# Optimization experiments

Hardware: AMD Instinct MI355X
Metric: run time of the kernel (lower is better)

Reference implementation:

```python
import jax, jax.numpy as jnp
import numpy as np

H = 512
V = 8000

def _attn(hidden, enc, W, b, v):
    # hidden: [1,B,H], enc: [T,B,H] -> context [1,B,H]
    encB = jnp.transpose(enc, (1, 0, 2))                      # [B,T,H]
    Hrep = jnp.broadcast_to(jnp.transpose(hidden, (1, 0, 2)), encB.shape)
    energy = jnp.tanh(jnp.concatenate([Hrep, encB], axis=-1) @ W.T + b)  # [B,T,H]
    scores = jnp.einsum('bth,h->bt', energy, v)               # [B,T]
    a = jax.nn.softmax(scores, axis=1)
    ctx = jnp.einsum('bt,bth->bh', a, encB)                   # [B,H]
    return ctx[None]

def _gru_step(x, h, W_ih, W_hh, b_ih, b_hh):
    # x: [B,in], h: [B,H]; PyTorch gate order r,z,n
    gi = x @ W_ih.T + b_ih
    gh = h @ W_hh.T + b_hh
    i_r, i_z, i_n = jnp.split(gi, 3, axis=1)
    h_r, h_z, h_n = jnp.split(gh, 3, axis=1)
    r = jax.nn.sigmoid(i_r + h_r)
    z = jax.nn.sigmoid(i_z + h_z)
    n = jnp.tanh(i_n + r * h_n)
    return (1.0 - z) * n + z * h

def setup_inputs() -> dict:
    key = jax.random.key(0)
    ks = jax.random.split(key, 20)
    B, Tz, Tu, E, D = 128, 64, 128, 512, 5
    gin = E + 2 * H + D  # 1541
    s = 0.02  # small init scale to keep tanh/sigmoid unsaturated
    return {
        'z_enc_out': jax.random.normal(ks[0], (Tz, B, H), jnp.float32),
        'u_enc_out': jax.random.normal(ks[1], (Tu, B, H), jnp.float32),
        'm_t_input': jax.random.randint(ks[2], (1, B), 0, V),
        'degree_input': jax.random.uniform(ks[3], (B, D), jnp.float32),
        'last_hidden': jax.random.normal(ks[4], (1, B, H), jnp.float32),
        'sparse_response': jax.random.uniform(ks[5], (B, Tz, V + Tz), jnp.float32, 1e-3, 1.0),
        'emb_table': jax.random.normal(ks[6], (V, E), jnp.float32) * s,
        'attn_z_W': jax.random.normal(ks[7], (H, 2 * H), jnp.float32) * s,
        'attn_z_b': jnp.zeros((H,), jnp.float32),
        'attn_z_v': jax.random.normal(ks[8], (H,), jnp.float32) * s,
        'attn_u_W': jax.random.normal(ks[9], (H, 2 * H), jnp.float32) * s,
        'attn_u_b': jnp.zeros((H,), jnp.float32),
        'attn_u_v': jax.random.normal(ks[10], (H,), jnp.float32) * s,
        'gru_W_ih': jax.random.normal(ks[11], (3 * H, gin), jnp.float32) * s,
        'gru_W_hh': jax.random.normal(ks[12], (3 * H, H), jnp.float32) * s,
        'gru_b_ih': jnp.zeros((3 * H,), jnp.float32),
        'gru_b_hh': jnp.zeros((3 * H,), jnp.float32),
        'proj_W': jax.random.normal(ks[13], (V, 3 * H), jnp.float32) * s,
        'proj_b': jnp.zeros((V,), jnp.float32),
        'copy2_W': jax.random.normal(ks[14], (H, H), jnp.float32) * s,
        'copy2_b': jnp.zeros((H,), jnp.float32),
    }

def reference(z_enc_out, u_enc_out, m_t_input, degree_input, last_hidden,
              sparse_response, emb_table, attn_z_W, attn_z_b, attn_z_v,
              attn_u_W, attn_u_b, attn_u_v, gru_W_ih, gru_W_hh, gru_b_ih,
              gru_b_hh, proj_W, proj_b, copy2_W, copy2_b):
    m_embed = emb_table[m_t_input]                                 # [1,B,E]
    z_ctx = _attn(last_hidden, z_enc_out, attn_z_W, attn_z_b, attn_z_v)  # [1,B,H]
    u_ctx = _attn(last_hidden, u_enc_out, attn_u_W, attn_u_b, attn_u_v)  # [1,B,H]
    gru_in = jnp.concatenate([m_embed, u_ctx, z_ctx, degree_input[None]], axis=2)
    h_new = _gru_step(gru_in[0], last_hidden[0], gru_W_ih, gru_W_hh, gru_b_ih, gru_b_hh)  # [B,H]
    gru_out = h_new[None]                                          # [1,B,H]
    gen_score = (jnp.concatenate([z_ctx, u_ctx, gru_out], axis=2)[0] @ proj_W.T + proj_b)  # [B,V]
    # copy scores over z encoder positions
    zT = jnp.transpose(z_enc_out, (1, 0, 2))                       # [B,Tz,H]
    cs = jnp.tanh(zT @ copy2_W.T + copy2_b)                        # [B,Tz,H]
    z_score = jnp.einsum('bth,bh->bt', cs, h_new)                  # [B,Tz]
    m = jnp.max(z_score, axis=1, keepdims=True)
    e = jnp.exp(z_score - m)
    z_copy = jnp.log(jnp.einsum('bt,btv->bv', e, sparse_response)) + m  # [B,V+Tz]
    scores = jax.nn.softmax(jnp.concatenate([gen_score, z_copy], axis=1), axis=1)
    gen, cp = scores[:, :V], scores[:, V:]
    proba = jnp.concatenate([gen + cp[:, :V], cp[:, V:]], axis=1)  # [B,V+Tz]
    return proba, gru_out, gru_out
```

## Files before the change

### kernel.cpp

```cpp
#include <hip/hip_runtime.h>
#include <hip/hip_bf16.h>
#include <math.h>

#define B_   128
#define H_   512
#define TZ   64
#define TU   128
#define V_   8000
#define VC   8064
#define GIN  1541
#define GINP 1568
#define G3   1536
#define NB   8

typedef float f32x4 __attribute__((ext_vector_type(4)));
typedef __bf16 bf16x8 __attribute__((ext_vector_type(8)));

__device__ __forceinline__ float sigmoidf_(float x){ return 1.f/(1.f+__expf(-x)); }

__device__ __forceinline__ void cvt8(const float* __restrict__ s, __bf16* __restrict__ d){
  float4 x = *(const float4*)s;
  float4 y = *(const float4*)(s+4);
  bf16x8 r;
  r[0]=(__bf16)x.x; r[1]=(__bf16)x.y; r[2]=(__bf16)x.z; r[3]=(__bf16)x.w;
  r[4]=(__bf16)y.x; r[5]=(__bf16)y.y; r[6]=(__bf16)y.z; r[7]=(__bf16)y.w;
  *(bf16x8*)d = r;
}

#define U_Z   524288u
#define U_U   1048576u
#define U_H   8192u
#define U_ZW  65536u
#define U_UW  65536u
#define U_CW  32768u
#define U_WHH 98304u
#define U_PW  1536000u
#define U_WIH 301056u
#define CVT_UNITS (U_Z+U_U+U_H+U_ZW+U_UW+U_CW+U_WHH+U_PW+U_WIH)

__global__ __launch_bounds__(256) void cvt_all(
    const float* __restrict__ z, const float* __restrict__ u, const float* __restrict__ hid,
    const float* __restrict__ zW, const float* __restrict__ uW, const float* __restrict__ cW,
    const float* __restrict__ whh, const float* __restrict__ pW, const float* __restrict__ wih,
    __bf16* __restrict__ zb, __bf16* __restrict__ ub, __bf16* __restrict__ hb,
    __bf16* __restrict__ zWb, __bf16* __restrict__ uWb, __bf16* __restrict__ cWb,
    __bf16* __restrict__ whhb, __bf16* __restrict__ pWb, __bf16* __restrict__ Wp)
{
  unsigned t = blockIdx.x*256u + threadIdx.x;
  if (t >= CVT_UNITS) return;
  unsigned o = t;
  if (o >= CVT_UNITS - U_WIH) {
    o -= (CVT_UNITS - U_WIH);
    unsigned r = o / (GINP/8), cu = o % (GINP/8);
    int c0 = cu*8;
    const float* src = wih + (size_t)r*GIN;
    bf16x8 v;
#pragma unroll
    for (int e = 0; e < 8; ++e) {
      int c = c0 + e;
      v[e] = (__bf16)((c < GIN) ? src[c] : 0.f);
    }
    *(bf16x8*)(Wp + (size_t)r*GINP + c0) = v;
    return;
  }
  const float* s; __bf16* d;
  if      (o < U_Z)                   { s=z;   d=zb;   }
  else if ((o-=U_Z)   < U_U)          { s=u;   d=ub;   }
  else if ((o-=U_U)   < U_H)          { s=hid; d=hb;   }
  else if ((o-=U_H)   < U_ZW)         { s=zW;  d=zWb;  }
  else if ((o-=U_ZW)  < U_UW)         { s=uW;  d=uWb;  }
  else if ((o-=U_UW)  < U_CW)         { s=cW;  d=cWb;  }
  else if ((o-=U_CW)  < U_WHH)        { s=whh; d=whhb; }
  else     { o-=U_WHH;                  s=pW;  d=pWb;  }
  cvt8(s + (size_t)o*8, d + (size_t)o*8);
}

__global__ __launch_bounds__(256) void hidden3(
    const __bf16* __restrict__ hb,
    const __bf16* __restrict__ zWb, const float* __restrict__ zbias, float* __restrict__ hWz,
    const __bf16* __restrict__ uWb, const float* __restrict__ ubias, float* __restrict__ hWu,
    const __bf16* __restrict__ whhb, const float* __restrict__ hbias, float* __restrict__ gh)
{
  const int wv = threadIdx.x >> 6, lane = threadIdx.x & 63;
  const int tile = blockIdx.x*4 + wv;
  if (tile >= 80) return;
  const __bf16* W; const float* bias; float* C; int ldw, ldc, nbn, lt;
  if (tile < 16)      { W=zWb;  bias=zbias; C=hWz; ldw=2*H_; ldc=H_; nbn=8;  lt=tile; }
  else if (tile < 32) { W=uWb;  bias=ubias; C=hWu; ldw=2*H_; ldc=H_; nbn=8;  lt=tile-16; }
  else                { W=whhb; bias=hbias; C=gh;  ldw=H_;   ldc=G3; nbn=24; lt=tile-32; }
  const int bn = (lt % nbn) * 64, bm = (lt / nbn) * 64;
  const int col = lane & 15, g = lane >> 4;
  f32x4 acc[4][4] = {};
  for (int k0 = 0; k0 < 512; k0 += 32) {
    const int k = k0 + g*8;
    bf16x8 af[4], bw[4];
#pragma unroll
    for (int i = 0; i < 4; ++i) {
      af[i] = *(const bf16x8*)(hb + (size_t)(bm + i*16 + col)*H_ + k);
      bw[i] = *(const bf16x8*)(W  + (size_t)(bn + i*16 + col)*ldw + k);
    }
#pragma unroll
    for (int i = 0; i < 4; ++i)
#pragma unroll
      for (int j = 0; j < 4; ++j)
        acc[i][j] = __builtin_amdgcn_mfma_f32_16x16x32_bf16(af[i], bw[j], acc[i][j], 0, 0, 0);
  }
#pragma unroll
  for (int mi = 0; mi < 4; ++mi)
#pragma unroll
    for (int r = 0; r < 4; ++r) {
      int m = bm + mi*16 + g*4 + r;
#pragma unroll
      for (int ni = 0; ni < 4; ++ni) {
        int n = bn + ni*16 + col;
        C[(size_t)m*ldc + n] = acc[mi][ni][r] + bias[n];
      }
    }
}

__global__ __launch_bounds__(256) void mfma_energy2(
    const __bf16* __restrict__ Az, const __bf16* __restrict__ Wz, int ldwz,
    const float* __restrict__ addz, int asz, const float* __restrict__ mulz, int msz,
    float* __restrict__ outz, int Tz,
    const __bf16* __restrict__ Au, const __bf16* __restrict__ Wu, int ldwu,
    const float* __restrict__ addu, int asu, const float* __restrict__ mulu, int msu,
    float* __restrict__ outu, int Tu,
    int ztiles, int ntiles)
{
  const int wv = threadIdx.x >> 6, lane = threadIdx.x & 63;
  const int tile = blockIdx.x*4 + wv;
  if (tile >= ntiles) return;
  const __bf16 *A, *W; const float *add, *mul; float* outp;
  int ldw, as, ms, T, lt;
  if (tile < ztiles) { A=Az; W=Wz; ldw=ldwz; add=addz; as=asz; mul=mulz; ms=msz; outp=outz; T=Tz; lt=tile; }
  else               { A=Au; W=Wu; ldw=ldwu; add=addu; as=asu; mul=mulu; ms=msu; outp=outu; T=Tu; lt=tile-ztiles; }
  const int nb = lt & 7;
  const int bn = nb * 64, bm = (lt >> 3) * 64;
  const int col = lane & 15, g = lane >> 4;
  f32x4 acc[4][4] = {};
  for (int k0 = 0; k0 < 512; k0 += 32) {
    const int k = k0 + g*8;
    bf16x8 af[4], bw[4];
#pragma unroll
    for (int i = 0; i < 4; ++i) {
      af[i] = *(const bf16x8*)(A + (size_t)(bm + i*16 + col)*512 + k);
      bw[i] = *(const bf16x8*)(W + (size_t)(bn + i*16 + col)*ldw + k);
    }
#pragma unroll
    for (int i = 0; i < 4; ++i)
#pragma unroll
      for (int j = 0; j < 4; ++j)
        acc[i][j] = __builtin_amdgcn_mfma_f32_16x16x32_bf16(af[i], bw[j], acc[i][j], 0, 0, 0);
  }
#pragma unroll
  for (int mi = 0; mi < 4; ++mi)
#pragma unroll
    for (int r = 0; r < 4; ++r) {
      int m = bm + mi*16 + g*4 + r;
      int b = m & (B_-1), t = m >> 7;
      float p = 0.f;
#pragma unroll
      for (int ni = 0; ni < 4; ++ni) {
        int n = bn + ni*16 + col;
        float v = tanhf(acc[mi][ni][r] + add[(size_t)b*as + n]);
        p += v * mul[(size_t)b*ms + n];
      }
      p += __shfl_xor(p, 1); p += __shfl_xor(p, 2);
      p += __shfl_xor(p, 4); p += __shfl_xor(p, 8);
      if (col == 0) outp[(size_t)nb*(B_*T) + b*T + t] = p;
    }
}

__global__ __launch_bounds__(256) void attn_ctx_concat(
    const float* __restrict__ partZ, const float* __restrict__ partU,
    const __bf16* __restrict__ zb, const __bf16* __restrict__ ub,
    const int* __restrict__ m_t, const float* __restrict__ emb,
    const float* __restrict__ degree,
    __bf16* __restrict__ gin, __bf16* __restrict__ cat3b)
{
  const int b = blockIdx.x, tid = threadIdx.x;
  __shared__ float sa[256];
  __shared__ float awz[TZ];
  __shared__ float awu[TU];
  {
    float s = -INFINITY;
    if (tid < TZ) {
      s = 0.f;
#pragma unroll
      for (int nb = 0; nb < NB; ++nb) s += partZ[(size_t)nb*(B_*TZ) + b*TZ + tid];
    }
    sa[tid] = s; __syncthreads();
    for (int o = 128; o > 0; o >>= 1) { if (tid < o) sa[tid] = fmaxf(sa[tid], sa[tid+o]); __syncthreads(); }
    float mx = sa[0]; __syncthreads();
    float e = (tid < TZ) ? __expf(s - mx) : 0.f;
    sa[tid] = e; __syncthreads();
    for (int o = 128; o > 0; o >>= 1) { if (tid < o) sa[tid] += sa[tid+o]; __syncthreads(); }
    float inv = 1.f / sa[0];
    if (tid < TZ) awz[tid] = e * inv;
    __syncthreads();
  }
  {
    float s = -INFINITY;
    if (tid < TU) {
      s = 0.f;
#pragma unroll
      for (int nb = 0; nb < NB; ++nb) s += partU[(size_t)nb*(B_*TU) + b*TU + tid];
    }
    sa[tid] = s; __syncthreads();
    for (int o = 128; o > 0; o >>= 1) { if (tid < o) sa[tid] = fmaxf(sa[tid], sa[tid+o]); __syncthreads(); }
    float mx = sa[0]; __syncthreads();
    float e = (tid < TU) ? __expf(s - mx) : 0.f;
    sa[tid] = e; __syncthreads();
    for (int o = 128; o > 0; o >>= 1) { if (tid < o) sa[tid] += sa[tid+o]; __syncthreads(); }
    float inv = 1.f / sa[0];
    if (tid < TU) awu[tid] = e * inv;
    __syncthreads();
  }
  const float* e = emb + (size_t)m_t[b] * H_;
  for (int h = tid; h < H_; h += 256) {
    float accz = 0.f, accu = 0.f;
    for (int t = 0; t < TZ; ++t) accz += awz[t] * (float)zb[((size_t)t*B_ + b)*H_ + h];
    for (int t = 0; t < TU; ++t) accu += awu[t] * (float)ub[((size_t)t*B_ + b)*H_ + h];
    gin[(size_t)b*GINP + h]          = (__bf16)e[h];
    gin[(size_t)b*GINP + H_ + h]     = (__bf16)accu;
    gin[(size_t)b*GINP + 2*H_ + h]   = (__bf16)accz;
    cat3b[(size_t)b*G3 + h]          = (__bf16)accz;
    cat3b[(size_t)b*G3 + H_ + h]     = (__bf16)accu;
  }
  if (tid < 5) gin[(size_t)b*GINP + 3*H_ + tid] = (__bf16)degree[b*5 + tid];
  if (tid >= 5 && tid < 32) gin[(size_t)b*GINP + GIN + (tid-5)] = (__bf16)0.f;
}

__global__ __launch_bounds__(256) void mfma_gru(
    const __bf16* __restrict__ A, const __bf16* __restrict__ W,
    float* __restrict__ giA, float* __restrict__ giB)
{
  const int wv = threadIdx.x >> 6, lane = threadIdx.x & 63;
  const int tile = blockIdx.x*4 + wv;
  if (tile >= 96) return;
  const int half = tile / 48, lt = tile % 48;
  const int bn = (lt % 24) * 64, bm = (lt / 24) * 64;
  const int col = lane & 15, g = lane >> 4;
  const int kbeg = half ? 800 : 0, kend_ = half ? GINP : 800;
  float* C = half ? giB : giA;
  f32x4 acc[4][4] = {};
  for (int k0 = kbeg; k0 < kend_; k0 += 32) {
    const int k = k0 + g*8;
    bf16x8 af[4], bw[4];
#pragma unroll
    for (int i = 0; i < 4; ++i) {
      af[i] = *(const bf16x8*)(A + (size_t)(bm + i*16 + col)*GINP + k);
      bw[i] = *(const bf16x8*)(W + (size_t)(bn + i*16 + col)*GINP + k);
    }
#pragma unroll
    for (int i = 0; i < 4; ++i)
#pragma unroll
      for (int j = 0; j < 4; ++j)
        acc[i][j] = __builtin_amdgcn_mfma_f32_16x16x32_bf16(af[i], bw[j], acc[i][j], 0, 0, 0);
  }
#pragma unroll
  for (int mi = 0; mi < 4; ++mi)
#pragma unroll
    for (int r = 0; r < 4; ++r) {
      int m = bm + mi*16 + g*4 + r;
#pragma unroll
      for (int ni = 0; ni < 4; ++ni)
        C[(size_t)m*G3 + bn + ni*16 + col] = acc[mi][ni][r];
    }
}

__global__ __launch_bounds__(256) void gru_kernel(
    const float* __restrict__ giA, const float* __restrict__ giB,
    const float* __restrict__ gh, const float* __restrict__ bih,
    const float* __restrict__ hprev,
    float* __restrict__ hnew, __bf16* __restrict__ cat3b,
    float* __restrict__ out1, float* __restrict__ out2)
{
  int idx = blockIdx.x*256 + threadIdx.x;
  int b = idx >> 9, h = idx & (H_-1);
  size_t base = (size_t)b*G3;
  float ir = giA[base + h]        + giB[base + h]        + bih[h]        + gh[base + h];
  float iz = giA[base + H_ + h]   + giB[base + H_ + h]   + bih[H_ + h]   + gh[base + H_ + h];
  float in_= giA[base + 2*H_ + h] + giB[base + 2*H_ + h] + bih[2*H_ + h];
  float hn = gh[base + 2*H_ + h];
  float r = sigmoidf_(ir);
  float z = sigmoidf_(iz);
  float n = tanhf(in_ + r*hn);
  float hv = (1.f - z)*n + z*hprev[idx];
  hnew[idx] = hv;
  cat3b[base + 2*H_ + h] = (__bf16)hv;
  out1[idx] = hv;
  out2[idx] = hv;
}

__global__ __launch_bounds__(256) void proj_copy(
    const __bf16* __restrict__ cat3b, const __bf16* __restrict__ pWb, float* __restrict__ P,
    const __bf16* __restrict__ zb, const __bf16* __restrict__ cWb,
    const float* __restrict__ c2b, const float* __restrict__ hnew,
    float* __restrict__ partC)
{
  const int wv = threadIdx.x >> 6, lane = threadIdx.x & 63;
  const int tile = blockIdx.x*4 + wv;
  const int col = lane & 15, g = lane >> 4;
  if (tile < 750) {
    const int s = tile / 250, t2 = tile % 250;
    const int bn = (t2 % 125) * 64, bm = (t2 / 125) * 64;
    const __bf16* As = cat3b + s*512;
    const __bf16* Ws = pWb + s*512;
    float* C = P + (size_t)s*B_*V_;
    f32x4 acc[4][4] = {};
    for (int k0 = 0; k0 < 512; k0 += 32) {
      const int k = k0 + g*8;
      bf16x8 af[4], bw[4];
#pragma unroll
      for (int i = 0; i < 4; ++i) {
        af[i] = *(const bf16x8*)(As + (size_t)(bm + i*16 + col)*G3 + k);
        bw[i] = *(const bf16x8*)(Ws + (size_t)(bn + i*16 + col)*G3 + k);
      }
#pragma unroll
      for (int i = 0; i < 4; ++i)
#pragma unroll
        for (int j = 0; j < 4; ++j)
          acc[i][j] = __builtin_amdgcn_mfma_f32_16x16x32_bf16(af[i], bw[j], acc[i][j], 0, 0, 0);
    }
#pragma unroll
    for (int mi = 0; mi < 4; ++mi)
#pragma unroll
      for (int r = 0; r < 4; ++r) {
        int m = bm + mi*16 + g*4 + r;
#pragma unroll
        for (int ni = 0; ni < 4; ++ni)
          C[(size_t)m*V_ + bn + ni*16 + col] = acc[mi][ni][r];
      }
  } else if (tile < 750 + 1024) {
    const int lt = tile - 750;
    const int nb = lt & 7;
    const int bn = nb * 64, bm = (lt >> 3) * 64;
    f32x4 acc[4][4] = {};
    for (int k0 = 0; k0 < 512; k0 += 32) {
      const int k = k0 + g*8;
      bf16x8 af[4], bw[4];
#pragma unroll
      for (int i = 0; i < 4; ++i) {
        af[i] = *(const bf16x8*)(zb + (size_t)(bm + i*16 + col)*512 + k);
        bw[i] = *(const bf16x8*)(cWb + (size_t)(bn + i*16 + col)*H_ + k);
      }
#pragma unroll
      for (int i = 0; i < 4; ++i)
#pragma unroll
        for (int j = 0; j < 4; ++j)
          acc[i][j] = __builtin_amdgcn_mfma_f32_16x16x32_bf16(af[i], bw[j], acc[i][j], 0, 0, 0);
    }
#pragma unroll
    for (int mi = 0; mi < 4; ++mi)
#pragma unroll
      for (int r = 0; r < 4; ++r) {
        int m = bm + mi*16 + g*4 + r;
        int b = m & (B_-1), t = m >> 7;
        float p = 0.f;
#pragma unroll
        for (int ni = 0; ni < 4; ++ni) {
          int n = bn + ni*16 + col;
          float v = tanhf(acc[mi][ni][r] + c2b[n]);
          p += v * hnew[(size_t)b*H_ + n];
        }
        p += __shfl_xor(p, 1); p += __shfl_xor(p, 2);
        p += __shfl_xor(p, 4); p += __shfl_xor(p, 8);
        if (col == 0) partC[(size_t)nb*(B_*TZ) + b*TZ + t] = p;
      }
  }
}

__global__ __launch_bounds__(256) void zcopy_kernel(
    const float* __restrict__ partC, const float* __restrict__ sr,
    float* __restrict__ zbuf)
{
  const int b = blockIdx.y, tid = threadIdx.x;
  __shared__ float se[TZ];
  __shared__ float smx;
  if (tid < TZ) {
    float s = 0.f;
#pragma unroll
    for (int nb = 0; nb < NB; ++nb) s += partC[(size_t)nb*(B_*TZ) + b*TZ + tid];
    float mx = s;
    mx = fmaxf(mx, __shfl_xor(mx, 1));  mx = fmaxf(mx, __shfl_xor(mx, 2));
    mx = fmaxf(mx, __shfl_xor(mx, 4));  mx = fmaxf(mx, __shfl_xor(mx, 8));
    mx = fmaxf(mx, __shfl_xor(mx, 16)); mx = fmaxf(mx, __shfl_xor(mx, 32));
    se[tid] = __expf(s - mx);
    if (tid == 0) smx = mx;
  }
  __syncthreads();
  const int v0 = blockIdx.x*1024 + tid*4;
  if (v0 >= VC) return;
  float4 acc = {0.f, 0.f, 0.f, 0.f};
  const float* base = sr + (size_t)b*TZ*VC;
#pragma unroll 4
  for (int t = 0; t < TZ; ++t) {
    float et = se[t];
    float4 x = *(const float4*)(base + (size_t)t*VC + v0);
    acc.x += et*x.x; acc.y += et*x.y; acc.z += et*x.z; acc.w += et*x.w;
  }
  float m = smx;
  float* out = zbuf + (size_t)b*VC + v0;
  out[0] = __logf(acc.x) + m;
  out[1] = __logf(acc.y) + m;
  out[2] = __logf(acc.z) + m;
  out[3] = __logf(acc.w) + m;
}

__global__ __launch_bounds__(256) void final_softmax2(
    const float* __restrict__ p0, const float* __restrict__ p1, const float* __restrict__ p2,
    const float* __restrict__ bias, const float* __restrict__ zbuf, float* __restrict__ out0)
{
  const int b = blockIdx.x, tid = threadIdx.x;
  const float* q0 = p0 + (size_t)b*V_;
  const float* q1 = p1 + (size_t)b*V_;
  const float* q2 = p2 + (size_t)b*V_;
  const float* zr = zbuf + (size_t)b*VC;
  __shared__ float sa[256];
  float mx = -INFINITY;
  for (int i = tid; i < V_; i += 256) mx = fmaxf(mx, q0[i]+q1[i]+q2[i]+bias[i]);
  for (int i = tid; i < VC; i += 256) mx = fmaxf(mx, zr[i]);
  sa[tid] = mx; __syncthreads();
  for (int o = 128; o > 0; o >>= 1) { if (tid < o) sa[tid] = fmaxf(sa[tid], sa[tid+o]); __syncthreads(); }
  mx = sa[0]; __syncthreads();
  float sum = 0.f;
  for (int i = tid; i < V_; i += 256) sum += __expf(q0[i]+q1[i]+q2[i]+bias[i] - mx);
  for (int i = tid; i < VC; i += 256) sum += __expf(zr[i] - mx);
  sa[tid] = sum; __syncthreads();
  for (int o = 128; o > 0; o >>= 1) { if (tid < o) sa[tid] += sa[tid+o]; __syncthreads(); }
  float inv = 1.f / sa[0];
  float* o0 = out0 + (size_t)b*VC;
  for (int j = tid; j < V_; j += 256)
    o0[j] = (__expf(q0[j]+q1[j]+q2[j]+bias[j]-mx) + __expf(zr[j]-mx)) * inv;
  for (int j = tid; j < TZ; j += 256)
    o0[V_ + j] = __expf(zr[V_ + j] - mx) * inv;
}

extern "C" void kernel_launch(void* const* d_in, const int* in_sizes, int n_in,
                              void* d_out, int out_size, void* d_ws, size_t ws_size,
                              hipStream_t stream)
{
  const float* z_enc   = (const float*)d_in[0];
  const float* u_enc   = (const float*)d_in[1];
  const int*   m_t     = (const int*)  d_in[2];
  const float* degree  = (const float*)d_in[3];
  const float* hidden  = (const float*)d_in[4];
  const float* sr      = (const float*)d_in[5];
  const float* emb     = (const float*)d_in[6];
  const float* attn_z_W= (const float*)d_in[7];
  const float* attn_z_b= (const float*)d_in[8];
  const float* attn_z_v= (const float*)d_in[9];
  const float* attn_u_W= (const float*)d_in[10];
  const float* attn_u_b= (const float*)d_in[11];
  const float* attn_u_v= (const float*)d_in[12];
  const float* gru_W_ih= (const float*)d_in[13];
  const float* gru_W_hh= (const float*)d_in[14];
  const float* gru_b_ih= (const float*)d_in[15];
  const float* gru_b_hh= (const float*)d_in[16];
  const float* proj_W  = (const float*)d_in[17];
  const float* proj_b  = (const float*)d_in[18];
  const float* copy2_W = (const float*)d_in[19];
  const float* copy2_b = (const float*)d_in[20];

  float* out0 = (float*)d_out;
  float* out1 = out0 + (size_t)B_*VC;
  float* out2 = out1 + (size_t)B_*H_;

  float* ws    = (float*)d_ws;
  float* hWz   = ws;
  float* hWu   = hWz   + B_*H_;
  float* gh    = hWu   + B_*H_;
  float* partZ = gh    + B_*G3;
  float* partU = partZ + NB*B_*TZ;
  float* partC = partU + NB*B_*TU;
  float* giA   = partC + NB*B_*TZ;
  float* giB   = giA   + B_*G3;
  float* hnew  = giB   + B_*G3;
  float* p0    = hnew  + B_*H_;
  float* p1    = p0    + (size_t)B_*V_;
  float* p2    = p1    + (size_t)B_*V_;
  float* zbuf  = p2    + (size_t)B_*V_;
  __bf16* gin   = (__bf16*)(zbuf + (size_t)B_*VC);
  __bf16* Wp    = gin   + (size_t)B_*GINP;
  __bf16* zb    = Wp    + (size_t)G3*GINP;
  __bf16* ub    = zb    + (size_t)TZ*B_*H_;
  __bf16* hb    = ub    + (size_t)TU*B_*H_;
  __bf16* zWb   = hb    + (size_t)B_*H_;
  __bf16* uWb   = zWb   + (size_t)H_*2*H_;
  __bf16* cWb   = uWb   + (size_t)H_*2*H_;
  __bf16* whhb  = cWb   + (size_t)H_*H_;
  __bf16* pWb   = whhb  + (size_t)G3*H_;
  __bf16* cat3b = pWb   + (size_t)V_*G3;

  cvt_all<<<(CVT_UNITS + 255)/256, 256, 0, stream>>>(
      z_enc, u_enc, hidden, attn_z_W, attn_u_W, copy2_W, gru_W_hh, proj_W, gru_W_ih,
      zb, ub, hb, zWb, uWb, cWb, whhb, pWb, Wp);

  hidden3<<<20, 256, 0, stream>>>(hb, zWb, attn_z_b, hWz, uWb, attn_u_b, hWu, whhb, gru_b_hh, gh);

  mfma_energy2<<<768, 256, 0, stream>>>(
      zb, zWb + H_, 2*H_, hWz, H_, attn_z_v, 0, partZ, TZ,
      ub, uWb + H_, 2*H_, hWu, H_, attn_u_v, 0, partU, TU,
      1024, 3072);

  attn_ctx_concat<<<B_, 256, 0, stream>>>(partZ, partU, zb, ub, m_t, emb, degree, gin, cat3b);

  mfma_gru<<<24, 256, 0, stream>>>(gin, Wp, giA, giB);
  gru_kernel<<<(B_*H_)/256, 256, 0, stream>>>(giA, giB, gh, gru_b_ih, hidden, hnew, cat3b, out1, out2);

  proj_copy<<<444, 256, 0, stream>>>(cat3b, pWb, p0, zb, cWb, copy2_b, hnew, partC);

  zcopy_kernel<<<dim3((VC + 1023)/1024, B_), 256, 0, stream>>>(partC, sr, zbuf);

  final_softmax2<<<B_, 256, 0, stream>>>(p0, p1, p2, proj_b, zbuf, out0);
}
```

Measured before the change: 295.2 us.

## Drop proj_W bf16 pre-conversion, stage energy A tiles in LDS, online softmax

Removes the separate fp32-to-bf16 conversion of the large projection weight and instead converts it inline while loading inside proj_copy. Each projection wave now covers all 128 batch rows, so every weight element is read once. The attention energy kernel stages a 64-row A tile in swizzled LDS that four waves share across 8 column blocks, cutting redundant global reads. The final softmax now makes a single online max/sum pass instead of separate max and sum passes. The trade-offs are more registers per wave in proj_copy (8x4 accumulators) and fewer waves in flight.

```diff
diff --git a/kernel.cpp b/kernel.cpp
--- a/kernel.cpp
+++ b/kernel.cpp
@@ -18,13 +18,16 @@
 
 __device__ __forceinline__ float sigmoidf_(float x){ return 1.f/(1.f+__expf(-x)); }
 
-__device__ __forceinline__ void cvt8(const float* __restrict__ s, __bf16* __restrict__ d){
-  float4 x = *(const float4*)s;
-  float4 y = *(const float4*)(s+4);
+__device__ __forceinline__ bf16x8 load8_bf16(const float* __restrict__ p){
+  float4 x = *(const float4*)p;
+  float4 y = *(const float4*)(p+4);
   bf16x8 r;
   r[0]=(__bf16)x.x; r[1]=(__bf16)x.y; r[2]=(__bf16)x.z; r[3]=(__bf16)x.w;
   r[4]=(__bf16)y.x; r[5]=(__bf16)y.y; r[6]=(__bf16)y.z; r[7]=(__bf16)y.w;
-  *(bf16x8*)d = r;
+  return r;
+}
+__device__ __forceinline__ void cvt8(const float* __restrict__ s, __bf16* __restrict__ d){
+  *(bf16x8*)d = load8_bf16(s);
 }
 
 #define U_Z   524288u
@@ -34,17 +37,16 @@
 #define U_UW  65536u
 #define U_CW  32768u
 #define U_WHH 98304u
-#define U_PW  1536000u
 #define U_WIH 301056u
-#define CVT_UNITS (U_Z+U_U+U_H+U_ZW+U_UW+U_CW+U_WHH+U_PW+U_WIH)
+#define CVT_UNITS (U_Z+U_U+U_H+U_ZW+U_UW+U_CW+U_WHH+U_WIH)
 
 __global__ __launch_bounds__(256) void cvt_all(
     const float* __restrict__ z, const float* __restrict__ u, const float* __restrict__ hid,
     const float* __restrict__ zW, const float* __restrict__ uW, const float* __restrict__ cW,
-    const float* __restrict__ whh, const float* __restrict__ pW, const float* __restrict__ wih,
+    const float* __restrict__ whh, const float* __restrict__ wih,
     __bf16* __restrict__ zb, __bf16* __restrict__ ub, __bf16* __restrict__ hb,
     __bf16* __restrict__ zWb, __bf16* __restrict__ uWb, __bf16* __restrict__ cWb,
-    __bf16* __restrict__ whhb, __bf16* __restrict__ pWb, __bf16* __restrict__ Wp)
+    __bf16* __restrict__ whhb, __bf16* __restrict__ Wp)
 {
   unsigned t = blockIdx.x*256u + threadIdx.x;
   if (t >= CVT_UNITS) return;
@@ -70,8 +72,7 @@
   else if ((o-=U_H)   < U_ZW)         { s=zW;  d=zWb;  }
   else if ((o-=U_ZW)  < U_UW)         { s=uW;  d=uWb;  }
   else if ((o-=U_UW)  < U_CW)         { s=cW;  d=cWb;  }
-  else if ((o-=U_CW)  < U_WHH)        { s=whh; d=whhb; }
-  else     { o-=U_WHH;                  s=pW;  d=pWb;  }
+  else     { o-=U_CW;                   s=whh; d=whhb; }
   cvt8(s + (size_t)o*8, d + (size_t)o*8);
 }
 
@@ -118,57 +119,72 @@
     }
 }
 
-__global__ __launch_bounds__(256) void mfma_energy2(
-    const __bf16* __restrict__ Az, const __bf16* __restrict__ Wz, int ldwz,
-    const float* __restrict__ addz, int asz, const float* __restrict__ mulz, int msz,
-    float* __restrict__ outz, int Tz,
-    const __bf16* __restrict__ Au, const __bf16* __restrict__ Wu, int ldwu,
-    const float* __restrict__ addu, int asu, const float* __restrict__ mulu, int msu,
-    float* __restrict__ outu, int Tu,
-    int ztiles, int ntiles)
-{
-  const int wv = threadIdx.x >> 6, lane = threadIdx.x & 63;
-  const int tile = blockIdx.x*4 + wv;
-  if (tile >= ntiles) return;
-  const __bf16 *A, *W; const float *add, *mul; float* outp;
-  int ldw, as, ms, T, lt;
-  if (tile < ztiles) { A=Az; W=Wz; ldw=ldwz; add=addz; as=asz; mul=mulz; ms=msz; outp=outz; T=Tz; lt=tile; }
-  else               { A=Au; W=Wu; ldw=ldwu; add=addu; as=asu; mul=mulu; ms=msu; outp=outu; T=Tu; lt=tile-ztiles; }
-  const int nb = lt & 7;
-  const int bn = nb * 64, bm = (lt >> 3) * 64;
+__global__ __launch_bounds__(256) void energy_lds(
+    const __bf16* __restrict__ zb, const __bf16* __restrict__ zWe,
+    const float* __restrict__ hWz, const float* __restrict__ vz, float* __restrict__ partZ,
+    const __bf16* __restrict__ ub, const __bf16* __restrict__ uWe,
+    const float* __restrict__ hWu, const float* __restrict__ vu, float* __restrict__ partU)
+{
+  __shared__ __bf16 Asm[64*512];
+  const int blk = blockIdx.x;
+  const __bf16 *A, *W; const float *add, *vv; float* outp; int T, bm;
+  if (blk < 128) { A=zb; W=zWe; add=hWz; vv=vz; outp=partZ; T=TZ; bm=blk*64; }
+  else           { A=ub; W=uWe; add=hWu; vv=vu; outp=partU; T=TU; bm=(blk-128)*64; }
+  const int tid = threadIdx.x;
+  {
+    const int r4 = tid >> 6;
+    const int c8 = (tid & 63) * 8;
+#pragma unroll
+    for (int it = 0; it < 16; ++it) {
+      int row = it*4 + r4;
+      unsigned off = (unsigned)row*1024u + (unsigned)c8*2u;
+      off ^= ((unsigned)(row & 7) << 4);
+      *(bf16x8*)((char*)Asm + off) = *(const bf16x8*)(A + (size_t)(bm + row)*512 + c8);
+    }
+  }
+  __syncthreads();
+  const int wv = tid >> 6, lane = tid & 63;
   const int col = lane & 15, g = lane >> 4;
-  f32x4 acc[4][4] = {};
-  for (int k0 = 0; k0 < 512; k0 += 32) {
-    const int k = k0 + g*8;
-    bf16x8 af[4], bw[4];
-#pragma unroll
-    for (int i = 0; i < 4; ++i) {
-      af[i] = *(const bf16x8*)(A + (size_t)(bm + i*16 + col)*512 + k);
-      bw[i] = *(const bf16x8*)(W + (size_t)(bn + i*16 + col)*ldw + k);
-    }
-#pragma unroll
-    for (int i = 0; i < 4; ++i)
-#pragma unroll
-      for (int j = 0; j < 4; ++j)
-        acc[i][j] = __builtin_amdgcn_mfma_f32_16x16x32_bf16(af[i], bw[j], acc[i][j], 0, 0, 0);
-  }
-#pragma unroll
-  for (int mi = 0; mi < 4; ++mi)
-#pragma unroll
-    for (int r = 0; r < 4; ++r) {
-      int m = bm + mi*16 + g*4 + r;
-      int b = m & (B_-1), t = m >> 7;
-      float p = 0.f;
-#pragma unroll
-      for (int ni = 0; ni < 4; ++ni) {
-        int n = bn + ni*16 + col;
-        float v = tanhf(acc[mi][ni][r] + add[(size_t)b*as + n]);
-        p += v * mul[(size_t)b*ms + n];
+#pragma unroll
+  for (int half = 0; half < 2; ++half) {
+    const int nb = wv + half*4;
+    const int bn = nb*64;
+    f32x4 acc[4][4] = {};
+    for (int k0 = 0; k0 < 512; k0 += 32) {
+      const int k = k0 + g*8;
+      bf16x8 af[4], bw[4];
+#pragma unroll
+      for (int i = 0; i < 4; ++i) {
+        int row = i*16 + col;
+        unsigned off = (unsigned)row*1024u + (unsigned)k*2u;
+        off ^= ((unsigned)(row & 7) << 4);
+        af[i] = *(const bf16x8*)((const char*)Asm + off);
+        bw[i] = *(const bf16x8*)(W + (size_t)(bn + i*16 + col)*(2*H_) + k);
       }
-      p += __shfl_xor(p, 1); p += __shfl_xor(p, 2);
-      p += __shfl_xor(p, 4); p += __shfl_xor(p, 8);
-      if (col == 0) outp[(size_t)nb*(B_*T) + b*T + t] = p;
-    }
+#pragma unroll
+      for (int i = 0; i < 4; ++i)
+#pragma unroll
+        for (int j = 0; j < 4; ++j)
+          acc[i][j] = __builtin_amdgcn_mfma_f32_16x16x32_bf16(af[i], bw[j], acc[i][j], 0, 0, 0);
+    }
+#pragma unroll
+    for (int mi = 0; mi < 4; ++mi)
+#pragma unroll
+      for (int r = 0; r < 4; ++r) {
+        int m = bm + mi*16 + g*4 + r;
+        int b = m & (B_-1), t = m >> 7;
+        float p = 0.f;
+#pragma unroll
+        for (int ni = 0; ni < 4; ++ni) {
+          int n = bn + ni*16 + col;
+          float v = tanhf(acc[mi][ni][r] + add[(size_t)b*H_ + n]);
+          p += v * vv[n];
+        }
+        p += __shfl_xor(p, 1); p += __shfl_xor(p, 2);
+        p += __shfl_xor(p, 4); p += __shfl_xor(p, 8);
+        if (col == 0) outp[(size_t)nb*(B_*T) + b*T + t] = p;
+      }
+  }
 }
 
 __global__ __launch_bounds__(256) void attn_ctx_concat(
@@ -294,7 +310,7 @@
 }
 
 __global__ __launch_bounds__(256) void proj_copy(
-    const __bf16* __restrict__ cat3b, const __bf16* __restrict__ pWb, float* __restrict__ P,
+    const __bf16* __restrict__ cat3b, const float* __restrict__ pW, float* __restrict__ P,
     const __bf16* __restrict__ zb, const __bf16* __restrict__ cWb,
     const float* __restrict__ c2b, const float* __restrict__ hnew,
     float* __restrict__ partC)
@@ -302,38 +318,39 @@
   const int wv = threadIdx.x >> 6, lane = threadIdx.x & 63;
   const int tile = blockIdx.x*4 + wv;
   const int col = lane & 15, g = lane >> 4;
-  if (tile < 750) {
-    const int s = tile / 250, t2 = tile % 250;
-    const int bn = (t2 % 125) * 64, bm = (t2 / 125) * 64;
+  if (tile < 375) {
+    const int s = tile / 125;
+    const int bn = (tile % 125) * 64;
     const __bf16* As = cat3b + s*512;
-    const __bf16* Ws = pWb + s*512;
+    const float*  Ws = pW + s*512;
     float* C = P + (size_t)s*B_*V_;
-    f32x4 acc[4][4] = {};
+    f32x4 acc[8][4] = {};
     for (int k0 = 0; k0 < 512; k0 += 32) {
       const int k = k0 + g*8;
-      bf16x8 af[4], bw[4];
-#pragma unroll
-      for (int i = 0; i < 4; ++i) {
-        af[i] = *(const bf16x8*)(As + (size_t)(bm + i*16 + col)*G3 + k);
-        bw[i] = *(const bf16x8*)(Ws + (size_t)(bn + i*16 + col)*G3 + k);
-      }
+      bf16x8 af[8], bw[4];
+#pragma unroll
+      for (int i = 0; i < 8; ++i)
+        af[i] = *(const bf16x8*)(As + (size_t)(i*16 + col)*G3 + k);
 #pragma unroll
       for (int i = 0; i < 4; ++i)
-#pragma unroll
-        for (int j = 0; j < 4; ++j)
-          acc[i][j] = __builtin_amdgcn_mfma_f32_16x16x32_bf16(af[i], bw[j], acc[i][j], 0, 0, 0);
-    }
-#pragma unroll
-    for (int mi = 0; mi < 4; ++mi)
+        bw[i] = load8_bf16(Ws + (size_t)(bn + i*16 + col)*G3 + k);
+#pragma unroll
+      for (int mi = 0; mi < 8; ++mi)
+#pragma unroll
+        for (int ni = 0; ni < 4; ++ni)
+          acc[mi][ni] = __builtin_amdgcn_mfma_f32_16x16x32_bf16(af[mi], bw[ni], acc[mi][ni], 0, 0, 0);
+    }
+#pragma unroll
+    for (int mi = 0; mi < 8; ++mi)
 #pragma unroll
       for (int r = 0; r < 4; ++r) {
-        int m = bm + mi*16 + g*4 + r;
+        int m = mi*16 + g*4 + r;
 #pragma unroll
         for (int ni = 0; ni < 4; ++ni)
           C[(size_t)m*V_ + bn + ni*16 + col] = acc[mi][ni][r];
       }
-  } else if (tile < 750 + 1024) {
-    const int lt = tile - 750;
+  } else if (tile < 375 + 1024) {
+    const int lt = tile - 375;
     const int nb = lt & 7;
     const int bn = nb * 64, bm = (lt >> 3) * 64;
     f32x4 acc[4][4] = {};
@@ -417,24 +434,34 @@
   const float* q1 = p1 + (size_t)b*V_;
   const float* q2 = p2 + (size_t)b*V_;
   const float* zr = zbuf + (size_t)b*VC;
-  __shared__ float sa[256];
-  float mx = -INFINITY;
-  for (int i = tid; i < V_; i += 256) mx = fmaxf(mx, q0[i]+q1[i]+q2[i]+bias[i]);
-  for (int i = tid; i < VC; i += 256) mx = fmaxf(mx, zr[i]);
-  sa[tid] = mx; __syncthreads();
-  for (int o = 128; o > 0; o >>= 1) { if (tid < o) sa[tid] = fmaxf(sa[tid], sa[tid+o]); __syncthreads(); }
-  mx = sa[0]; __syncthreads();
-  float sum = 0.f;
-  for (int i = tid; i < V_; i += 256) sum += __expf(q0[i]+q1[i]+q2[i]+bias[i] - mx);
-  for (int i = tid; i < VC; i += 256) sum += __expf(zr[i] - mx);
-  sa[tid] = sum; __syncthreads();
-  for (int o = 128; o > 0; o >>= 1) { if (tid < o) sa[tid] += sa[tid+o]; __syncthreads(); }
-  float inv = 1.f / sa[0];
+  float m = -INFINITY, s = 0.f;
+  for (int i = tid; i < V_; i += 256) {
+    float v = q0[i]+q1[i]+q2[i]+bias[i];
+    if (v > m) { s = s*__expf(m - v) + 1.f; m = v; }
+    else       { s += __expf(v - m); }
+  }
+  for (int i = tid; i < VC; i += 256) {
+    float v = zr[i];
+    if (v > m) { s = s*__expf(m - v) + 1.f; m = v; }
+    else       { s += __expf(v - m); }
+  }
+  __shared__ float sm[256], ss[256];
+  sm[tid] = m; ss[tid] = s; __syncthreads();
+  for (int o = 128; o > 0; o >>= 1) {
+    if (tid < o) {
+      float m2 = sm[tid+o], s2 = ss[tid+o];
+      float M = fmaxf(sm[tid], m2);
+      ss[tid] = ss[tid]*__expf(sm[tid]-M) + s2*__expf(m2-M);
+      sm[tid] = M;
+    }
+    __syncthreads();
+  }
+  float MX = sm[0], inv = 1.f / ss[0];
   float* o0 = out0 + (size_t)b*VC;
   for (int j = tid; j < V_; j += 256)
-    o0[j] = (__expf(q0[j]+q1[j]+q2[j]+bias[j]-mx) + __expf(zr[j]-mx)) * inv;
+    o0[j] = (__expf(q0[j]+q1[j]+q2[j]+bias[j]-MX) + __expf(zr[j]-MX)) * inv;
   for (int j = tid; j < TZ; j += 256)
-    o0[V_ + j] = __expf(zr[V_ + j] - mx) * inv;
+    o0[V_ + j] = __expf(zr[V_ + j] - MX) * inv;
 }
 
 extern "C" void kernel_launch(void* const* d_in, const int* in_sizes, int n_in,
@@ -490,26 +517,24 @@
   __bf16* uWb   = zWb   + (size_t)H_*2*H_;
   __bf16* cWb   = uWb   + (size_t)H_*2*H_;
   __bf16* whhb  = cWb   + (size_t)H_*H_;
-  __bf16* pWb   = whhb  + (size_t)G3*H_;
-  __bf16* cat3b = pWb   + (size_t)V_*G3;
+  __bf16* cat3b = whhb  + (size_t)G3*H_;
 
   cvt_all<<<(CVT_UNITS + 255)/256, 256, 0, stream>>>(
-      z_enc, u_enc, hidden, attn_z_W, attn_u_W, copy2_W, gru_W_hh, proj_W, gru_W_ih,
-      zb, ub, hb, zWb, uWb, cWb, whhb, pWb, Wp);
+      z_enc, u_enc, hidden, attn_z_W, attn_u_W, copy2_W, gru_W_hh, gru_W_ih,
+      zb, ub, hb, zWb, uWb, cWb, whhb, Wp);
 
   hidden3<<<20, 256, 0, stream>>>(hb, zWb, attn_z_b, hWz, uWb, attn_u_b, hWu, whhb, gru_b_hh, gh);
 
-  mfma_energy2<<<768, 256, 0, stream>>>(
-      zb, zWb + H_, 2*H_, hWz, H_, attn_z_v, 0, partZ, TZ,
-      ub, uWb + H_, 2*H_, hWu, H_, attn_u_v, 0, partU, TU,
-      1024, 3072);
+  energy_lds<<<384, 256, 0, stream>>>(
+      zb, zWb + H_, hWz, attn_z_v, partZ,
+      ub, uWb + H_, hWu, attn_u_v, partU);
 
   attn_ctx_concat<<<B_, 256, 0, stream>>>(partZ, partU, zb, ub, m_t, emb, degree, gin, cat3b);
 
   mfma_gru<<<24, 256, 0, stream>>>(gin, Wp, giA, giB);
   gru_kernel<<<(B_*H_)/256, 256, 0, stream>>>(giA, giB, gh, gru_b_ih, hidden, hnew, cat3b, out1, out2);
 
-  proj_copy<<<444, 256, 0, stream>>>(cat3b, pWb, p0, zb, cWb, copy2_b, hnew, partC);
+  proj_copy<<<350, 256, 0, stream>>>(cat3b, proj_W, p0, zb, cWb, copy2_b, hnew, partC);
 
   zcopy_kernel<<<dim3((VC + 1023)/1024, B_), 256, 0, stream>>>(partC, sr, zbuf);
 
```

New measurement: 327.7 us. 11.0% more time.
